# Performance work log

Hardware: AMD Instinct MI355X
Metric: run time of the kernel (lower is better)

## Reference

```python
import jax, jax.numpy as jnp
import numpy as np

SEP_TOKEN_ID = 102
B, S, H = 64, 512, 1024


def setup_inputs() -> dict:
    key = jax.random.key(0)
    k1, k2 = jax.random.split(key)
    hidden_states = jax.random.normal(k1, (B, S, H), dtype=jnp.float32)
    input_ids = jax.random.randint(k2, (B, S), 0, 200, dtype=jnp.int64)
    return {"hidden_states": hidden_states, "input_ids": input_ids}


def _segment_pools(hidden_states, input_ids):
    # hidden_states: [B, S, H], input_ids: [B, S]
    b, s, h = hidden_states.shape
    pos = jnp.arange(s)  # [S]
    sep = input_ids == SEP_TOKEN_ID  # [B, S] bool
    n_sep = sep.sum(axis=1)  # [B]
    has_sep = n_sep >= 1  # [B]
    first_sep = jnp.argmax(sep, axis=1)  # [B], 0 if no sep (gated by has_sep)
    last_sep = s - 1 - jnp.argmax(sep[:, ::-1], axis=1)  # [B]

    # title segment: tokens in [1, first_sep); empty unless first_sep > 1
    title_mask = (pos[None, :] >= 1) & (pos[None, :] < first_sep[:, None]) & has_sep[:, None]

    # lead segment: (first_sep, last_sep) if >=2 seps, else (first_sep, SeqLen)
    lead_end = jnp.where(n_sep >= 2, last_sep, s)  # [B]
    lead_mask = (pos[None, :] > first_sep[:, None]) & (pos[None, :] < lead_end[:, None]) & has_sep[:, None]

    def masked_mean(mask):
        m = mask.astype(hidden_states.dtype)  # [B, S]
        seg_sum = jnp.einsum('bs,bsh->bh', m, hidden_states)  # [B, H]
        cnt = m.sum(axis=1)  # [B]
        mean = seg_sum / jnp.maximum(cnt, 1.0)[:, None]
        return jnp.where(cnt[:, None] > 0, mean, 0.0)  # zeros for empty segments

    return masked_mean(title_mask), masked_mean(lead_mask)


def reference(hidden_states, input_ids):
    return _segment_pools(hidden_states, input_ids)
```

## Files before the change

kernel.cpp:

```cpp
#include <hip/hip_runtime.h>
#include <hip/hip_bf16.h>

#define SEP_ID 102
#define BB 64
#define SS 512
#define HH 1024

__device__ __forceinline__ void accum_range(const float* __restrict__ rb,
                                            int lo, int end, int wv,
                                            float4& a0, float4& a1)
{
    int s = lo + wv;
    for (; s + 48 < end; s += 64) {
        float4 v0 = *reinterpret_cast<const float4*>(rb + (size_t)(s     ) * HH);
        float4 v1 = *reinterpret_cast<const float4*>(rb + (size_t)(s + 16) * HH);
        float4 v2 = *reinterpret_cast<const float4*>(rb + (size_t)(s + 32) * HH);
        float4 v3 = *reinterpret_cast<const float4*>(rb + (size_t)(s + 48) * HH);
        a0.x += v0.x + v2.x;  a0.y += v0.y + v2.y;
        a0.z += v0.z + v2.z;  a0.w += v0.w + v2.w;
        a1.x += v1.x + v3.x;  a1.y += v1.y + v3.y;
        a1.z += v1.z + v3.z;  a1.w += v1.w + v3.w;
    }
    for (; s < end; s += 16) {
        float4 v = *reinterpret_cast<const float4*>(rb + (size_t)s * HH);
        a0.x += v.x; a0.y += v.y; a0.z += v.z; a0.w += v.w;
    }
}

__global__ __launch_bounds__(1024) void seg_pool_kernel(
    const float* __restrict__ hs,
    const int*   __restrict__ ids,
    float*       __restrict__ out)
{
    const int hq   = blockIdx.x;
    const int b    = blockIdx.y;
    const int tid  = threadIdx.x;
    const int lane = tid & 63;
    const int wv   = tid >> 6;

    __shared__ int s_first, s_last, s_cnt;
    if (tid == 0) { s_first = SS; s_last = -1; s_cnt = 0; }
    __syncthreads();
    if (tid < SS) {
        if (ids[b * SS + tid] == SEP_ID) {
            atomicMin(&s_first, tid);
            atomicMax(&s_last, tid);
            atomicAdd(&s_cnt, 1);
        }
    }
    __syncthreads();
    const int cnt      = s_cnt;
    const int has      = (cnt >= 1) ? 1 : 0;
    const int first    = has ? s_first : 0;
    const int lead_end = (cnt >= 2) ? s_last : SS;

    const float* rb = hs + (size_t)b * SS * HH + hq * 256 + lane * 4;

    float4 aT0 = make_float4(0.f,0.f,0.f,0.f), aT1 = make_float4(0.f,0.f,0.f,0.f);
    float4 aL0 = make_float4(0.f,0.f,0.f,0.f), aL1 = make_float4(0.f,0.f,0.f,0.f);

    const int tEnd = has ? first    : 0;
    const int lEnd = has ? lead_end : 0;
    accum_range(rb, 1,         tEnd, wv, aT0, aT1);
    accum_range(rb, first + 1, lEnd, wv, aL0, aL1);

    float4 aT = make_float4(aT0.x + aT1.x, aT0.y + aT1.y, aT0.z + aT1.z, aT0.w + aT1.w);
    float4 aL = make_float4(aL0.x + aL1.x, aL0.y + aL1.y, aL0.z + aL1.z, aL0.w + aL1.w);

    __shared__ float4 ldsT[16][64];
    __shared__ float4 ldsL[16][64];
    ldsT[wv][lane] = aT;
    ldsL[wv][lane] = aL;
    __syncthreads();

    if (wv == 0) {
        float4 sT = make_float4(0.f,0.f,0.f,0.f);
        #pragma unroll
        for (int j = 0; j < 16; ++j) {
            float4 a = ldsT[j][lane];
            sT.x += a.x; sT.y += a.y; sT.z += a.z; sT.w += a.w;
        }
        int cT = has ? (first - 1) : 0; if (cT < 0) cT = 0;
        float4 o;
        if (cT > 0) { float d = (float)cT; o = make_float4(sT.x/d, sT.y/d, sT.z/d, sT.w/d); }
        else        { o = make_float4(0.f,0.f,0.f,0.f); }
        *reinterpret_cast<float4*>(out + (size_t)b * HH + hq * 256 + lane * 4) = o;
    } else if (wv == 1) {
        float4 sL = make_float4(0.f,0.f,0.f,0.f);
        #pragma unroll
        for (int j = 0; j < 16; ++j) {
            float4 a = ldsL[j][lane];
            sL.x += a.x; sL.y += a.y; sL.z += a.z; sL.w += a.w;
        }
        int cL = has ? (lead_end - first - 1) : 0; if (cL < 0) cL = 0;
        float4 o;
        if (cL > 0) { float d = (float)cL; o = make_float4(sL.x/d, sL.y/d, sL.z/d, sL.w/d); }
        else        { o = make_float4(0.f,0.f,0.f,0.f); }
        *reinterpret_cast<float4*>(out + (size_t)BB * HH + (size_t)b * HH + hq * 256 + lane * 4) = o;
    }
}

extern "C" void kernel_launch(void* const* d_in, const int* in_sizes, int n_in,
                              void* d_out, int out_size, void* d_ws, size_t ws_size,
                              hipStream_t stream) {
    const float* hs = (const float*)d_in[0];
    const int*  ids = (const int*)d_in[1];
    float* out = (float*)d_out;

    dim3 grid(HH / 256, BB);
    seg_pool_kernel<<<grid, 1024, 0, stream>>>(hs, ids, out);
}
```

Before: 21.56 us.

## Split sequence into chunks across blocks with workspace partials and finalize pass

Replaces the single kernel, where each block reduced one 256-column slice over the whole sequence with 16 waves and an LDS reduction, with two kernels. In the first, each block handles one batch row, all 1024 columns and one sequence chunk of up to 16, writing title and lead partial sums to the workspace. The second kernel sums those partials and divides by the counts. The aim is better load balance and more blocks in flight, since the sequence chunks spread uneven segment lengths over many blocks. It costs a second launch, the workspace round trip, and a repeated SEP scan in every block.

```diff
diff --git a/kernel.cpp b/kernel.cpp
--- a/kernel.cpp
+++ b/kernel.cpp
@@ -6,98 +6,118 @@
 #define SS 512
 #define HH 1024
 
-__device__ __forceinline__ void accum_range(const float* __restrict__ rb,
-                                            int lo, int end, int wv,
-                                            float4& a0, float4& a1)
+__device__ __forceinline__ void accum_rows(const float* __restrict__ rb,
+                                           int lo, int end,
+                                           float4& a0, float4& a1)
 {
-    int s = lo + wv;
-    for (; s + 48 < end; s += 64) {
-        float4 v0 = *reinterpret_cast<const float4*>(rb + (size_t)(s     ) * HH);
-        float4 v1 = *reinterpret_cast<const float4*>(rb + (size_t)(s + 16) * HH);
-        float4 v2 = *reinterpret_cast<const float4*>(rb + (size_t)(s + 32) * HH);
-        float4 v3 = *reinterpret_cast<const float4*>(rb + (size_t)(s + 48) * HH);
+    int s = lo;
+    for (; s + 3 < end; s += 4) {
+        float4 v0 = *reinterpret_cast<const float4*>(rb + (size_t)(s    ) * HH);
+        float4 v1 = *reinterpret_cast<const float4*>(rb + (size_t)(s + 1) * HH);
+        float4 v2 = *reinterpret_cast<const float4*>(rb + (size_t)(s + 2) * HH);
+        float4 v3 = *reinterpret_cast<const float4*>(rb + (size_t)(s + 3) * HH);
         a0.x += v0.x + v2.x;  a0.y += v0.y + v2.y;
         a0.z += v0.z + v2.z;  a0.w += v0.w + v2.w;
         a1.x += v1.x + v3.x;  a1.y += v1.y + v3.y;
         a1.z += v1.z + v3.z;  a1.w += v1.w + v3.w;
     }
-    for (; s < end; s += 16) {
+    for (; s < end; ++s) {
         float4 v = *reinterpret_cast<const float4*>(rb + (size_t)s * HH);
         a0.x += v.x; a0.y += v.y; a0.z += v.z; a0.w += v.w;
     }
 }
 
-__global__ __launch_bounds__(1024) void seg_pool_kernel(
-    const float* __restrict__ hs,
-    const int*   __restrict__ ids,
-    float*       __restrict__ out)
+__device__ __forceinline__ void meta_scan(const int* __restrict__ ids, int b,
+                                          int t, int nthr,
+                                          int& first, int& lead_end, int& has)
 {
-    const int hq   = blockIdx.x;
-    const int b    = blockIdx.y;
-    const int tid  = threadIdx.x;
-    const int lane = tid & 63;
-    const int wv   = tid >> 6;
-
     __shared__ int s_first, s_last, s_cnt;
-    if (tid == 0) { s_first = SS; s_last = -1; s_cnt = 0; }
+    if (t == 0) { s_first = SS; s_last = -1; s_cnt = 0; }
     __syncthreads();
-    if (tid < SS) {
-        if (ids[b * SS + tid] == SEP_ID) {
-            atomicMin(&s_first, tid);
-            atomicMax(&s_last, tid);
+    for (int k = t; k < SS; k += nthr) {
+        if (ids[b * SS + k] == SEP_ID) {
+            atomicMin(&s_first, k);
+            atomicMax(&s_last, k);
             atomicAdd(&s_cnt, 1);
         }
     }
     __syncthreads();
-    const int cnt      = s_cnt;
-    const int has      = (cnt >= 1) ? 1 : 0;
-    const int first    = has ? s_first : 0;
-    const int lead_end = (cnt >= 2) ? s_last : SS;
+    int cnt  = s_cnt;
+    has      = (cnt >= 1) ? 1 : 0;
+    first    = has ? s_first : 0;
+    lead_end = (cnt >= 2) ? s_last : SS;
+}
 
-    const float* rb = hs + (size_t)b * SS * HH + hq * 256 + lane * 4;
+__global__ __launch_bounds__(256) void pool_kernel(
+    const float* __restrict__ hs,
+    const int*   __restrict__ ids,
+    float*       __restrict__ part,
+    int NS, int SC)
+{
+    const int id = blockIdx.x;
+    const int q  = id >> 6;
+    const int b  = ((id & 63) + q) & 63;
+    const int t  = threadIdx.x;
 
+    int first, lead_end, has;
+    meta_scan(ids, b, t, 256, first, lead_end, has);
+
+    const int s0 = q * SC;
+    const int s1 = (s0 + SC < SS) ? s0 + SC : SS;
+
+    int tlo = (s0 > 1) ? s0 : 1;
+    int thi = has ? ((first < s1) ? first : s1) : 0;
+    int llo = (s0 > first + 1) ? s0 : first + 1;
+    int lhi = has ? ((lead_end < s1) ? lead_end : s1) : 0;
+
+    const float* rb = hs + (size_t)b * SS * HH + t * 4;
     float4 aT0 = make_float4(0.f,0.f,0.f,0.f), aT1 = make_float4(0.f,0.f,0.f,0.f);
     float4 aL0 = make_float4(0.f,0.f,0.f,0.f), aL1 = make_float4(0.f,0.f,0.f,0.f);
+    accum_rows(rb, tlo, thi, aT0, aT1);
+    accum_rows(rb, llo, lhi, aL0, aL1);
 
-    const int tEnd = has ? first    : 0;
-    const int lEnd = has ? lead_end : 0;
-    accum_range(rb, 1,         tEnd, wv, aT0, aT1);
-    accum_range(rb, first + 1, lEnd, wv, aL0, aL1);
+    size_t base = ((size_t)id * 2) * HH + t * 4;
+    float4 oT = make_float4(aT0.x+aT1.x, aT0.y+aT1.y, aT0.z+aT1.z, aT0.w+aT1.w);
+    float4 oL = make_float4(aL0.x+aL1.x, aL0.y+aL1.y, aL0.z+aL1.z, aL0.w+aL1.w);
+    *reinterpret_cast<float4*>(part + base)      = oT;
+    *reinterpret_cast<float4*>(part + base + HH) = oL;
+}
 
-    float4 aT = make_float4(aT0.x + aT1.x, aT0.y + aT1.y, aT0.z + aT1.z, aT0.w + aT1.w);
-    float4 aL = make_float4(aL0.x + aL1.x, aL0.y + aL1.y, aL0.z + aL1.z, aL0.w + aL1.w);
+__global__ __launch_bounds__(256) void finalize_kernel(
+    const float* __restrict__ part,
+    const int*   __restrict__ ids,
+    float*       __restrict__ out,
+    int NS)
+{
+    const int b = blockIdx.x;
+    const int t = threadIdx.x;
 
-    __shared__ float4 ldsT[16][64];
-    __shared__ float4 ldsL[16][64];
-    ldsT[wv][lane] = aT;
-    ldsL[wv][lane] = aL;
-    __syncthreads();
+    int first, lead_end, has;
+    meta_scan(ids, b, t, 256, first, lead_end, has);
 
-    if (wv == 0) {
-        float4 sT = make_float4(0.f,0.f,0.f,0.f);
-        #pragma unroll
-        for (int j = 0; j < 16; ++j) {
-            float4 a = ldsT[j][lane];
-            sT.x += a.x; sT.y += a.y; sT.z += a.z; sT.w += a.w;
-        }
-        int cT = has ? (first - 1) : 0; if (cT < 0) cT = 0;
-        float4 o;
-        if (cT > 0) { float d = (float)cT; o = make_float4(sT.x/d, sT.y/d, sT.z/d, sT.w/d); }
-        else        { o = make_float4(0.f,0.f,0.f,0.f); }
-        *reinterpret_cast<float4*>(out + (size_t)b * HH + hq * 256 + lane * 4) = o;
-    } else if (wv == 1) {
-        float4 sL = make_float4(0.f,0.f,0.f,0.f);
-        #pragma unroll
-        for (int j = 0; j < 16; ++j) {
-            float4 a = ldsL[j][lane];
-            sL.x += a.x; sL.y += a.y; sL.z += a.z; sL.w += a.w;
-        }
-        int cL = has ? (lead_end - first - 1) : 0; if (cL < 0) cL = 0;
-        float4 o;
-        if (cL > 0) { float d = (float)cL; o = make_float4(sL.x/d, sL.y/d, sL.z/d, sL.w/d); }
-        else        { o = make_float4(0.f,0.f,0.f,0.f); }
-        *reinterpret_cast<float4*>(out + (size_t)BB * HH + (size_t)b * HH + hq * 256 + lane * 4) = o;
+    float4 sT = make_float4(0.f,0.f,0.f,0.f);
+    float4 sL = make_float4(0.f,0.f,0.f,0.f);
+    #pragma unroll 4
+    for (int q = 0; q < NS; ++q) {
+        int id = q * 64 + ((b - q) & 63);
+        size_t p = ((size_t)id * 2) * HH + t * 4;
+        float4 a = *reinterpret_cast<const float4*>(part + p);
+        float4 c = *reinterpret_cast<const float4*>(part + p + HH);
+        sT.x += a.x; sT.y += a.y; sT.z += a.z; sT.w += a.w;
+        sL.x += c.x; sL.y += c.y; sL.z += c.z; sL.w += c.w;
     }
+
+    int cT = has ? (first - 1) : 0;            if (cT < 0) cT = 0;
+    int cL = has ? (lead_end - first - 1) : 0; if (cL < 0) cL = 0;
+
+    float4 oT, oL;
+    if (cT > 0) { float d = (float)cT; oT = make_float4(sT.x/d, sT.y/d, sT.z/d, sT.w/d); }
+    else        { oT = make_float4(0.f,0.f,0.f,0.f); }
+    if (cL > 0) { float d = (float)cL; oL = make_float4(sL.x/d, sL.y/d, sL.z/d, sL.w/d); }
+    else        { oL = make_float4(0.f,0.f,0.f,0.f); }
+
+    *reinterpret_cast<float4*>(out + (size_t)b * HH + t * 4)                   = oT;
+    *reinterpret_cast<float4*>(out + (size_t)BB * HH + (size_t)b * HH + t * 4) = oL;
 }
 
 extern "C" void kernel_launch(void* const* d_in, const int* in_sizes, int n_in,
@@ -107,6 +127,11 @@
     const int*  ids = (const int*)d_in[1];
     float* out = (float*)d_out;
 
-    dim3 grid(HH / 256, BB);
-    seg_pool_kernel<<<grid, 1024, 0, stream>>>(hs, ids, out);
+    int NS = 16;
+    while (NS > 1 && (size_t)NS * 64 * 2 * HH * sizeof(float) > ws_size) NS >>= 1;
+    float* part = (float*)d_ws;
+
+    int SC = (SS + NS - 1) / NS;
+    pool_kernel<<<NS * 64, 256, 0, stream>>>(hs, ids, part, NS, SC);
+    finalize_kernel<<<BB, 256, 0, stream>>>(part, ids, out, NS);
 }
```

After: 26.72 us. 1.24x slower.
